# Kernel tuning notes

Hardware: AMD Instinct MI355X
Metric: run time of the kernel (lower is better)

## Reference

```python
import jax, jax.numpy as jnp
import numpy as np

EMB = 1024
HEADS = 16
HEAD_DIM = EMB // HEADS
FF = 4 * EMB


def _gelu_tanh(x):
    c = jnp.sqrt(jnp.asarray(2.0 / jnp.pi, x.dtype))
    return 0.5 * x * (1.0 + jnp.tanh(c * (x + 0.044715 * x ** 3)))


def _layernorm(x, scale, shift, eps=1e-5):
    mean = jnp.mean(x, axis=-1, keepdims=True)
    var = jnp.mean((x - mean) ** 2, axis=-1, keepdims=True)
    return scale * (x - mean) / jnp.sqrt(var + eps) + shift


def setup_inputs() -> dict:
    key = jax.random.key(0)
    ks = jax.random.split(key, 8)
    s = 0.02
    return {
        "x": jax.random.normal(ks[0], (2, 2048, EMB), jnp.float32),
        "w_q": jax.random.normal(ks[1], (EMB, EMB), jnp.float32) * s,
        "w_k": jax.random.normal(ks[2], (EMB, EMB), jnp.float32) * s,
        "w_v": jax.random.normal(ks[3], (EMB, EMB), jnp.float32) * s,
        "w_o": jax.random.normal(ks[4], (EMB, EMB), jnp.float32) * s,
        "b_o": jnp.zeros((EMB,), jnp.float32),
        "ln1_scale": jnp.ones((EMB,), jnp.float32),
        "ln1_shift": jnp.zeros((EMB,), jnp.float32),
        "ln2_scale": jnp.ones((EMB,), jnp.float32),
        "ln2_shift": jnp.zeros((EMB,), jnp.float32),
        "w_ff1": jax.random.normal(ks[5], (EMB, FF), jnp.float32) * s,
        "b_ff1": jnp.zeros((FF,), jnp.float32),
        "w_ff2": jax.random.normal(ks[6], (FF, EMB), jnp.float32) * s,
        "b_ff2": jnp.zeros((EMB,), jnp.float32),
    }


def _attention(x, w_q, w_k, w_v, w_o, b_o):
    b, n, _ = x.shape
    q = (x @ w_q).reshape(b, n, HEADS, HEAD_DIM).transpose(0, 2, 1, 3)  # bhnd
    k = (x @ w_k).reshape(b, n, HEADS, HEAD_DIM).transpose(0, 2, 1, 3)
    v = (x @ w_v).reshape(b, n, HEADS, HEAD_DIM).transpose(0, 2, 1, 3)
    scores = jnp.einsum("bhqd,bhkd->bhqk", q, k)
    causal = jnp.triu(jnp.ones((n, n), bool), k=1)
    scores = jnp.where(causal, -jnp.inf, scores)
    # original scales AFTER masking (-inf stays -inf)
    attn = jax.nn.softmax(scores / jnp.sqrt(jnp.asarray(HEAD_DIM, x.dtype)), axis=-1)
    ctx = jnp.einsum("bhqk,bhkd->bhqd", attn, v)
    ctx = ctx.transpose(0, 2, 1, 3).reshape(b, n, EMB)
    return ctx @ w_o + b_o


def reference(x, w_q, w_k, w_v, w_o, b_o, ln1_scale, ln1_shift,
              ln2_scale, ln2_shift, w_ff1, b_ff1, w_ff2, b_ff2):
    h = _layernorm(x, ln1_scale, ln1_shift)
    h = _attention(h, w_q, w_k, w_v, w_o, b_o)
    x = x + h  # dropout is identity at drop_rate=0 / eval
    h = _layernorm(x, ln2_scale, ln2_shift)
    h = _gelu_tanh(h @ w_ff1 + b_ff1) @ w_ff2 + b_ff2
    return x + h
```

## Files before the change

kernel.cpp:

```cpp
#include <hip/hip_runtime.h>
#include <math.h>

#define EMB 1024
#define HEADS 16
#define HD 64
#define FF_DIM 4096
#define SEQ 2048
#define BATCH 2
#define NTOK (BATCH * SEQ)

typedef __bf16 bf16x8 __attribute__((ext_vector_type(8)));
typedef float f32x4 __attribute__((ext_vector_type(4)));

__device__ __forceinline__ unsigned short f2bf(float f) {
    union { float f; unsigned int u; } v; v.f = f;
    unsigned int r = v.u + 0x7fff + ((v.u >> 16) & 1);
    return (unsigned short)(r >> 16);
}

__device__ __forceinline__ unsigned int cvt_pk_bf16(float a, float b) {
    unsigned int r;
    asm("v_cvt_pk_bf16_f32 %0, %1, %2" : "=v"(r) : "v"(a), "v"(b));
    return r;
}

__device__ __forceinline__ float gelu_f(float x) {
    const float A = 1.5957691216057308f;
    const float B = 0.07135481282989427f;
    float zz = x * (A + B * x * x);
    return x * __builtin_amdgcn_rcpf(1.f + __expf(-zz));
}

#define GLOAD_LDS16(g, l)                                                      \
    __builtin_amdgcn_global_load_lds(                                          \
        (const __attribute__((address_space(1))) void*)(g),                    \
        (__attribute__((address_space(3))) void*)(l), 16, 0, 0)

__global__ __launch_bounds__(256) void ln_kernel(const float* __restrict__ x,
                                                 const float* __restrict__ scale,
                                                 const float* __restrict__ shift,
                                                 unsigned short* __restrict__ out) {
    int row = blockIdx.x;
    const float* xr = x + (size_t)row * EMB;
    unsigned short* yr = out + (size_t)row * EMB;
    int t = threadIdx.x;

    float v[4];
    float s = 0.f, s2 = 0.f;
#pragma unroll
    for (int i = 0; i < 4; i++) {
        v[i] = xr[t + i * 256];
        s += v[i];
        s2 += v[i] * v[i];
    }
    for (int o = 32; o > 0; o >>= 1) {
        s += __shfl_down(s, o, 64);
        s2 += __shfl_down(s2, o, 64);
    }
    __shared__ float red[4], red2[4];
    int wave = t >> 6;
    if ((t & 63) == 0) { red[wave] = s; red2[wave] = s2; }
    __syncthreads();
    if (t == 0) {
        float a = 0.f, b = 0.f;
#pragma unroll
        for (int i = 0; i < 4; i++) { a += red[i]; b += red2[i]; }
        red[0] = a; red2[0] = b;
    }
    __syncthreads();
    float mean = red[0] * (1.f / EMB);
    float var = red2[0] * (1.f / EMB) - mean * mean;
    float rstd = rsqrtf(var + 1e-5f);
#pragma unroll
    for (int i = 0; i < 4; i++) {
        int c = t + i * 256;
        yr[c] = f2bf(scale[c] * (v[i] - mean) * rstd + shift[c]);
    }
}

__global__ __launch_bounds__(256) void prep_kernel(
    const float* __restrict__ w0, const float* __restrict__ w1,
    const float* __restrict__ w2, const float* __restrict__ w3,
    const float* __restrict__ w4, const float* __restrict__ w5,
    unsigned short* __restrict__ o0, unsigned short* __restrict__ o1,
    unsigned short* __restrict__ o2, unsigned short* __restrict__ o3,
    unsigned short* __restrict__ o4, unsigned short* __restrict__ o5,
    const float* __restrict__ x, const float* __restrict__ ln1s,
    const float* __restrict__ ln1b, unsigned short* __restrict__ lnO) {
    __shared__ float tile[64][65];
    __shared__ float red[4], red2[4];
    int id = blockIdx.x;
    int t = threadIdx.x;

    if (id >= 3072) {
        int row = id - 3072;
        const float* xr = x + (size_t)row * EMB;
        unsigned short* yr = lnO + (size_t)row * EMB;
        float v[4];
        float s = 0.f, s2 = 0.f;
#pragma unroll
        for (int i = 0; i < 4; i++) {
            v[i] = xr[t + i * 256];
            s += v[i];
            s2 += v[i] * v[i];
        }
        for (int o = 32; o > 0; o >>= 1) {
            s += __shfl_down(s, o, 64);
            s2 += __shfl_down(s2, o, 64);
        }
        int wave = t >> 6;
        if ((t & 63) == 0) { red[wave] = s; red2[wave] = s2; }
        __syncthreads();
        if (t == 0) {
            float a = 0.f, b = 0.f;
#pragma unroll
            for (int i = 0; i < 4; i++) { a += red[i]; b += red2[i]; }
            red[0] = a; red2[0] = b;
        }
        __syncthreads();
        float mean = red[0] * (1.f / EMB);
        float var = red2[0] * (1.f / EMB) - mean * mean;
        float rstd = rsqrtf(var + 1e-5f);
#pragma unroll
        for (int i = 0; i < 4; i++) {
            int c = t + i * 256;
            yr[c] = f2bf(ln1s[c] * (v[i] - mean) * rstd + ln1b[c]);
        }
        return;
    }

    const float* src; unsigned short* dst; int K, N, lid;
    if (id < 256)       { src = w0; dst = o0; K = 1024; N = 1024; lid = id; }
    else if (id < 512)  { src = w1; dst = o1; K = 1024; N = 1024; lid = id - 256; }
    else if (id < 768)  { src = w2; dst = o2; K = 1024; N = 1024; lid = id - 512; }
    else if (id < 1024) { src = w3; dst = o3; K = 1024; N = 1024; lid = id - 768; }
    else if (id < 2048) { src = w4; dst = o4; K = 1024; N = 4096; lid = id - 1024; }
    else                { src = w5; dst = o5; K = 4096; N = 1024; lid = id - 2048; }
    int tn = N >> 6;
    int k0 = (lid / tn) << 6, n0 = (lid % tn) << 6;
    int rr = t >> 6, cc = t & 63;
#pragma unroll
    for (int i = 0; i < 16; i++) {
        int r = i * 4 + rr;
        tile[r][cc] = src[(size_t)(k0 + r) * N + n0 + cc];
    }
    __syncthreads();
#pragma unroll
    for (int i = 0; i < 16; i++) {
        int r = i * 4 + rr;
        dst[(size_t)(n0 + r) * K + k0 + cc] = f2bf(tile[cc][r]);
    }
}


__global__ __launch_bounds__(256) void ff1_gemm(
    const unsigned short* __restrict__ A,
    const unsigned short* __restrict__ Bt,
    unsigned short* __restrict__ C,
    const float* __restrict__ bias,
    int M, int N, int K) {
    __shared__ unsigned short As[2][128 * 64];
    __shared__ unsigned short Bs[2][128 * 64];

    const int t = threadIdx.x;
    const int w = t >> 6, lane = t & 63;
    const int m0 = blockIdx.x * 128, n0 = blockIdx.y * 128;

    const int srow = lane >> 3;
    const int sc = (lane & 7) ^ srow;
    const unsigned short* gA[4];
    const unsigned short* gB[4];
#pragma unroll
    for (int i = 0; i < 4; i++) {
        gA[i] = A + (size_t)(m0 + i * 32 + w * 8 + srow) * K + sc * 8;
        gB[i] = Bt + (size_t)(n0 + i * 32 + w * 8 + srow) * K + sc * 8;
    }

    const int mrow = (w >> 1) * 64, ncol = (w & 1) * 64;
    int ph[2];
#pragma unroll
    for (int s = 0; s < 2; s++) ph[s] = ((s * 4 + (lane >> 4)) ^ (lane & 7)) * 8;
    int abase[4], bbase[4];
#pragma unroll
    for (int i = 0; i < 4; i++) {
        abase[i] = (mrow + i * 16 + (lane & 15)) * 64;
        bbase[i] = (ncol + i * 16 + (lane & 15)) * 64;
    }

    f32x4 acc[4][4];
#pragma unroll
    for (int i = 0; i < 4; i++)
#pragma unroll
        for (int j = 0; j < 4; j++) acc[i][j] = (f32x4){0.f, 0.f, 0.f, 0.f};

#define STG1(b)                                                                \
    do {                                                                       \
        _Pragma("unroll") for (int i_ = 0; i_ < 4; i_++) {                     \
            GLOAD_LDS16(gA[i_], &As[b][(i_ * 32 + w * 8) * 64]);               \
            GLOAD_LDS16(gB[i_], &Bs[b][(i_ * 32 + w * 8) * 64]);               \
            gA[i_] += 64; gB[i_] += 64;                                        \
        }                                                                      \
    } while (0)

    STG1(0);
    const int nk = K >> 6;
    for (int it = 0; it < nk; it++) {
        const int buf = it & 1;
        __syncthreads();
        if (it + 1 < nk) STG1(buf ^ 1);
#pragma unroll
        for (int s = 0; s < 2; s++) {
            bf16x8 af[4], bfr[4];
#pragma unroll
            for (int i = 0; i < 4; i++) {
                af[i] = *reinterpret_cast<const bf16x8*>(&As[buf][abase[i] + ph[s]]);
                bfr[i] = *reinterpret_cast<const bf16x8*>(&Bs[buf][bbase[i] + ph[s]]);
            }
#pragma unroll
            for (int i = 0; i < 4; i++)
#pragma unroll
                for (int j = 0; j < 4; j++)
                    acc[i][j] = __builtin_amdgcn_mfma_f32_16x16x32_bf16(
                        af[i], bfr[j], acc[i][j], 0, 0, 0);
        }
    }
#undef STG1

    const int ccol = lane & 15;
    const int crow = (lane >> 4) << 2;
#pragma unroll
    for (int i = 0; i < 4; i++) {
#pragma unroll
        for (int j = 0; j < 4; j++) {
            int col = n0 + ncol + j * 16 + ccol;
            float badd = bias[col];
#pragma unroll
            for (int r = 0; r < 4; r++) {
                int row = m0 + mrow + i * 16 + crow + r;
                C[(size_t)row * N + col] = f2bf(gelu_f(acc[i][j][r] + badd));
            }
        }
    }
}

__global__ __launch_bounds__(256) void ff2_gemm(
    const unsigned short* __restrict__ A,
    const unsigned short* __restrict__ Bt,
    float* __restrict__ C,
    const float* __restrict__ bias,
    int M, int N, int K) {
    __shared__ unsigned short As[2][128 * 64];
    __shared__ unsigned short Bs[2][128 * 64];

    const int t = threadIdx.x;
    const int w = t >> 6, lane = t & 63;
    const int id = blockIdx.x;
    const int n0 = (id & 7) * 128;
    const int ks = (id >> 3) & 1;
    const int m0 = (id >> 4) * 128;
    const int khalf = K >> 1;
    const int kbeg = ks * khalf;

    const int srow = lane >> 3;
    const int sc = (lane & 7) ^ srow;
    const unsigned short* gA[4];
    const unsigned short* gB[4];
#pragma unroll
    for (int i = 0; i < 4; i++) {
        gA[i] = A + (size_t)(m0 + i * 32 + w * 8 + srow) * K + kbeg + sc * 8;
        gB[i] = Bt + (size_t)(n0 + i * 32 + w * 8 + srow) * K + kbeg + sc * 8;
    }

    const int mrow = (w >> 1) * 64, ncol = (w & 1) * 64;
    int ph[2];
#pragma unroll
    for (int s = 0; s < 2; s++) ph[s] = ((s * 4 + (lane >> 4)) ^ (lane & 7)) * 8;
    int abase[4], bbase[4];
#pragma unroll
    for (int i = 0; i < 4; i++) {
        abase[i] = (mrow + i * 16 + (lane & 15)) * 64;
        bbase[i] = (ncol + i * 16 + (lane & 15)) * 64;
    }

    f32x4 acc[4][4];
#pragma unroll
    for (int i = 0; i < 4; i++)
#pragma unroll
        for (int j = 0; j < 4; j++) acc[i][j] = (f32x4){0.f, 0.f, 0.f, 0.f};

#define STG2(b)                                                                \
    do {                                                                       \
        _Pragma("unroll") for (int i_ = 0; i_ < 4; i_++) {                     \
            GLOAD_LDS16(gA[i_], &As[b][(i_ * 32 + w * 8) * 64]);               \
            GLOAD_LDS16(gB[i_], &Bs[b][(i_ * 32 + w * 8) * 64]);               \
            gA[i_] += 64; gB[i_] += 64;                                        \
        }                                                                      \
    } while (0)

    STG2(0);
    const int nk = khalf >> 6;
    for (int it = 0; it < nk; it++) {
        const int buf = it & 1;
        __syncthreads();
        if (it + 1 < nk) STG2(buf ^ 1);
#pragma unroll
        for (int s = 0; s < 2; s++) {
            bf16x8 af[4], bfr[4];
#pragma unroll
            for (int i = 0; i < 4; i++) {
                af[i] = *reinterpret_cast<const bf16x8*>(&As[buf][abase[i] + ph[s]]);
                bfr[i] = *reinterpret_cast<const bf16x8*>(&Bs[buf][bbase[i] + ph[s]]);
            }
#pragma unroll
            for (int i = 0; i < 4; i++)
#pragma unroll
                for (int j = 0; j < 4; j++)
                    acc[i][j] = __builtin_amdgcn_mfma_f32_16x16x32_bf16(
                        af[i], bfr[j], acc[i][j], 0, 0, 0);
        }
    }
#undef STG2

    const int ccol = lane & 15;
    const int crow = (lane >> 4) << 2;
#pragma unroll
    for (int i = 0; i < 4; i++) {
#pragma unroll
        for (int j = 0; j < 4; j++) {
            int col = n0 + ncol + j * 16 + ccol;
            float badd = ks == 0 ? bias[col] : 0.f;
#pragma unroll
            for (int r = 0; r < 4; r++) {
                int row = m0 + mrow + i * 16 + crow + r;
                size_t idx = (size_t)row * N + col;
                unsafeAtomicAdd(&C[idx], acc[i][j][r] + badd);
            }
        }
    }
}

template <int EPI>
__global__ __launch_bounds__(256) void mfma_gemm_s64(
    const unsigned short* __restrict__ A,
    const unsigned short* __restrict__ Bt,
    float* __restrict__ C,
    const float* __restrict__ bias,
    const float* __restrict__ resid,
    int M, int N, int K) {
    __shared__ unsigned short As[2][64 * 64];
    __shared__ unsigned short Bs[2][64 * 64];

    const int t = threadIdx.x;
    const int w = t >> 6, lane = t & 63;
    const int m0 = blockIdx.x * 64, n0 = blockIdx.y * 64;

    const int srow = lane >> 3;
    const int sc = (lane & 7) ^ srow;
    const unsigned short* gA[2];
    const unsigned short* gB[2];
#pragma unroll
    for (int i = 0; i < 2; i++) {
        gA[i] = A + (size_t)(m0 + i * 32 + w * 8 + srow) * K + sc * 8;
        gB[i] = Bt + (size_t)(n0 + i * 32 + w * 8 + srow) * K + sc * 8;
    }

    int ph[2];
#pragma unroll
    for (int s = 0; s < 2; s++) ph[s] = ((s * 4 + (lane >> 4)) ^ (lane & 7)) * 8;
    const int mrow = (w >> 1) * 32, ncol = (w & 1) * 32;
    int abase[2], bbase[2];
#pragma unroll
    for (int i = 0; i < 2; i++) {
        abase[i] = (mrow + i * 16 + (lane & 15)) * 64;
        bbase[i] = (ncol + i * 16 + (lane & 15)) * 64;
    }

    f32x4 acc[2][2];
#pragma unroll
    for (int i = 0; i < 2; i++)
#pragma unroll
        for (int j = 0; j < 2; j++) acc[i][j] = (f32x4){0.f, 0.f, 0.f, 0.f};

#define STGS(b)                                                                \
    do {                                                                       \
        _Pragma("unroll") for (int i_ = 0; i_ < 2; i_++) {                     \
            GLOAD_LDS16(gA[i_], &As[b][(i_ * 32 + w * 8) * 64]);               \
            GLOAD_LDS16(gB[i_], &Bs[b][(i_ * 32 + w * 8) * 64]);               \
            gA[i_] += 64; gB[i_] += 64;                                        \
        }                                                                      \
    } while (0)

    STGS(0);
    const int nk = K >> 6;
    for (int it = 0; it < nk; it++) {
        const int buf = it & 1;
        __syncthreads();
        if (it + 1 < nk) STGS(buf ^ 1);
#pragma unroll
        for (int s = 0; s < 2; s++) {
            bf16x8 af[2], bfr[2];
#pragma unroll
            for (int i = 0; i < 2; i++) {
                af[i] = *reinterpret_cast<const bf16x8*>(&As[buf][abase[i] + ph[s]]);
                bfr[i] = *reinterpret_cast<const bf16x8*>(&Bs[buf][bbase[i] + ph[s]]);
            }
#pragma unroll
            for (int i = 0; i < 2; i++)
#pragma unroll
                for (int j = 0; j < 2; j++)
                    acc[i][j] = __builtin_amdgcn_mfma_f32_16x16x32_bf16(
                        af[i], bfr[j], acc[i][j], 0, 0, 0);
        }
    }
#undef STGS

    const int ccol = lane & 15;
    const int crow = (lane >> 4) << 2;
#pragma unroll
    for (int i = 0; i < 2; i++) {
#pragma unroll
        for (int j = 0; j < 2; j++) {
            int col = n0 + ncol + j * 16 + ccol;
            float badd = bias[col];
#pragma unroll
            for (int r = 0; r < 4; r++) {
                int row = m0 + mrow + i * 16 + crow + r;
                size_t idx = (size_t)row * N + col;
                if constexpr (EPI == 1) {
                    C[idx] = acc[i][j][r] + badd + resid[idx];
                } else {
                    C[idx] = C[idx] + acc[i][j][r] + badd;
                }
            }
        }
    }
}

__global__ __launch_bounds__(256) void qkv_gemm(
    const unsigned short* __restrict__ lnO,
    const unsigned short* __restrict__ wqkT,
    const unsigned short* __restrict__ wvT,
    unsigned short* __restrict__ q,
    unsigned short* __restrict__ kb,
    unsigned short* __restrict__ vT) {
    __shared__ unsigned short As[2][128 * 64];
    __shared__ unsigned short Bs[2][128 * 64];

    const int t = threadIdx.x;
    const int w = t >> 6, lane = t & 63;
    const int bid = blockIdx.x;
    const bool qk = bid < 512;

    const unsigned short *A, *Bt;
    int m0, n0, N;
    if (qk) {
        A = lnO; Bt = wqkT;
        m0 = (bid & 31) * 128; n0 = (bid >> 5) * 128; N = 2048;
    } else {
        int lb = bid - 512;
        A = wvT; Bt = lnO;
        m0 = (lb & 7) * 128; n0 = (lb >> 3) * 128; N = 4096;
    }
    const int K = 1024;

    const int srow = lane >> 3;
    const int sc = (lane & 7) ^ srow;
    const unsigned short* gA[4];
    const unsigned short* gB[4];
#pragma unroll
    for (int i = 0; i < 4; i++) {
        gA[i] = A + (size_t)(m0 + i * 32 + w * 8 + srow) * K + sc * 8;
        gB[i] = Bt + (size_t)(n0 + i * 32 + w * 8 + srow) * K + sc * 8;
    }

    const int mrow = (w >> 1) * 64, ncol = (w & 1) * 64;
    int ph[2];
#pragma unroll
    for (int s = 0; s < 2; s++) ph[s] = ((s * 4 + (lane >> 4)) ^ (lane & 7)) * 8;
    int abase[4], bbase[4];
#pragma unroll
    for (int i = 0; i < 4; i++) {
        abase[i] = (mrow + i * 16 + (lane & 15)) * 64;
        bbase[i] = (ncol + i * 16 + (lane & 15)) * 64;
    }

    f32x4 acc[4][4];
#pragma unroll
    for (int i = 0; i < 4; i++)
#pragma unroll
        for (int j = 0; j < 4; j++) acc[i][j] = (f32x4){0.f, 0.f, 0.f, 0.f};

#define STGQ(b)                                                                \
    do {                                                                       \
        _Pragma("unroll") for (int i_ = 0; i_ < 4; i_++) {                     \
            GLOAD_LDS16(gA[i_], &As[b][(i_ * 32 + w * 8) * 64]);               \
            GLOAD_LDS16(gB[i_], &Bs[b][(i_ * 32 + w * 8) * 64]);               \
            gA[i_] += 64; gB[i_] += 64;                                        \
        }                                                                      \
    } while (0)

    STGQ(0);
    const int nk = K >> 6;
    for (int it = 0; it < nk; it++) {
        const int buf = it & 1;
        __syncthreads();
        if (it + 1 < nk) STGQ(buf ^ 1);
#pragma unroll
        for (int s = 0; s < 2; s++) {
            bf16x8 af[4], bfr[4];
#pragma unroll
            for (int i = 0; i < 4; i++) {
                af[i] = *reinterpret_cast<const bf16x8*>(&As[buf][abase[i] + ph[s]]);
                bfr[i] = *reinterpret_cast<const bf16x8*>(&Bs[buf][bbase[i] + ph[s]]);
            }
#pragma unroll
            for (int i = 0; i < 4; i++)
#pragma unroll
                for (int j = 0; j < 4; j++)
                    acc[i][j] = __builtin_amdgcn_mfma_f32_16x16x32_bf16(
                        af[i], bfr[j], acc[i][j], 0, 0, 0);
        }
    }
#undef STGQ

    const int ccol = lane & 15;
    const int crow = (lane >> 4) << 2;
    unsigned short* dst;
    int nbase;
    if (qk) {
        dst = (n0 < 1024) ? q : kb;
        nbase = n0 & 1023;
    } else {
        dst = vT;
        nbase = n0;
    }
    const int ldc = qk ? 1024 : 4096;
#pragma unroll
    for (int i = 0; i < 4; i++) {
#pragma unroll
        for (int j = 0; j < 4; j++) {
            int col = nbase + ncol + j * 16 + ccol;
#pragma unroll
            for (int r = 0; r < 4; r++) {
                int row = m0 + mrow + i * 16 + crow + r;
                dst[(size_t)row * ldc + col] = f2bf(acc[i][j][r]);
            }
        }
    }
}

__global__ __launch_bounds__(256) void attn_mfma(
    const unsigned short* __restrict__ Q,
    const unsigned short* __restrict__ K,
    const unsigned short* __restrict__ Vt,
    unsigned short* __restrict__ O) {
    __shared__ unsigned short Ks[2][64 * 64];
    __shared__ unsigned short Vs[2][64 * 64];
    __shared__ unsigned short Ps[4][16 * 64];

    const int t = threadIdx.x;
    const int w = t >> 6, lane = t & 63;
    const int l15 = lane & 15, l4 = lane >> 4;
    const int bh = blockIdx.x;
    const int b = bh >> 4, h = bh & 15;
    const int pair = blockIdx.y;

    const int sr = (w << 3) + (lane >> 3);
    const int sc = lane & 7;
    const int c = sc ^ (sr & 7);
    const unsigned short* kbase = K + ((size_t)(b * SEQ)) * EMB + h * HD;
    const unsigned short* vbase = Vt + ((size_t)(h * HD)) * (size_t)NTOK + (size_t)b * SEQ;
    unsigned short* Pw = &Ps[w][0];

#define STAGE(k0s, buf)                                                        \
    do {                                                                       \
        GLOAD_LDS16(kbase + (size_t)((k0s) + sr) * EMB + c * 8,                \
                    &Ks[buf][(w << 3) * 64]);                                  \
        GLOAD_LDS16(kbase + (size_t)((k0s) + sr + 32) * EMB + c * 8,           \
                    &Ks[buf][((w << 3) + 32) * 64]);                           \
        GLOAD_LDS16(vbase + (size_t)sr * NTOK + (k0s) + c * 8,                 \
                    &Vs[buf][(w << 3) * 64]);                                  \
        GLOAD_LDS16(vbase + (size_t)(sr + 32) * NTOK + (k0s) + c * 8,          \
                    &Vs[buf][((w << 3) + 32) * 64]);                           \
    } while (0)

    const float C1 = 0.125f * 1.4426950408889634f;
    const float C2 = 3.0f * 1.4426950408889634f;

#pragma unroll
    for (int phase = 0; phase < 2; phase++) {
        const int qt = phase ? pair : (31 - pair);
        const int q0 = qt * 64;

        const unsigned short* qg =
            Q + ((size_t)(b * SEQ + q0 + w * 16 + l15)) * EMB + h * HD + l4 * 8;
        bf16x8 qf0 = *(const bf16x8*)qg;
        bf16x8 qf1 = *(const bf16x8*)(qg + 32);
        const int qrow = q0 + w * 16 + l15;

        float ls[4] = {0.f, 0.f, 0.f, 0.f};
        f32x4 Oacc[4];
#pragma unroll
        for (int j = 0; j < 4; j++) Oacc[j] = (f32x4){0.f, 0.f, 0.f, 0.f};

        const int ntiles = qt + 1;
        __syncthreads();
        STAGE(0, 0);
        for (int tile = 0; tile < ntiles; tile++) {
            const int k0 = tile * 64;
            const int buf = tile & 1;
            __syncthreads();
            if (tile + 1 < ntiles) STAGE(k0 + 64, buf ^ 1);

            f32x4 S[4];
#pragma unroll
            for (int j = 0; j < 4; j++) S[j] = (f32x4){0.f, 0.f, 0.f, 0.f};
#pragma unroll
            for (int s = 0; s < 2; s++) {
                bf16x8 qf = s ? qf1 : qf0;
#pragma unroll
                for (int j = 0; j < 4; j++) {
                    int rk = 16 * j + l15;
                    int phys = (s * 4 + l4) ^ (rk & 7);
                    bf16x8 kf = *(const bf16x8*)&Ks[buf][rk * 64 + phys * 8];
                    S[j] = __builtin_amdgcn_mfma_f32_16x16x32_bf16(kf, qf, S[j], 0, 0, 0);
                }
            }

            if (tile == ntiles - 1) {
#pragma unroll
                for (int j = 0; j < 4; j++)
#pragma unroll
                    for (int r = 0; r < 4; r++) {
                        float e = exp2f(S[j][r] * C1 - C2);
                        if (k0 + 16 * j + 4 * l4 + r > qrow) e = 0.f;
                        S[j][r] = e;
                    }
            } else {
#pragma unroll
                for (int j = 0; j < 4; j++)
#pragma unroll
                    for (int r = 0; r < 4; r++)
                        S[j][r] = exp2f(S[j][r] * C1 - C2);
            }

#pragma unroll
            for (int j = 0; j < 4; j++) {
                ls[j] += S[j][0] + S[j][1] + S[j][2] + S[j][3];
                unsigned int lo = cvt_pk_bf16(S[j][0], S[j][1]);
                unsigned int hi = cvt_pk_bf16(S[j][2], S[j][3]);
                int chunk = (2 * j + (l4 >> 1)) ^ (l15 & 7);
                uint2 val; val.x = lo; val.y = hi;
                *reinterpret_cast<uint2*>(&Pw[l15 * 64 + chunk * 8 + (l4 & 1) * 4]) = val;
            }

#pragma unroll
            for (int s = 0; s < 2; s++) {
                int pch = (4 * s + l4) ^ (l15 & 7);
                bf16x8 pf = *(const bf16x8*)&Pw[l15 * 64 + pch * 8];
#pragma unroll
                for (int j = 0; j < 4; j++) {
                    int rv = 16 * j + l15;
                    int vph = (s * 4 + l4) ^ (rv & 7);
                    bf16x8 vf = *(const bf16x8*)&Vs[buf][rv * 64 + vph * 8];
                    Oacc[j] = __builtin_amdgcn_mfma_f32_16x16x32_bf16(vf, pf, Oacc[j], 0, 0, 0);
                }
            }
        }

        float l = ls[0] + ls[1] + ls[2] + ls[3];
        l += __shfl_xor(l, 16, 64);
        l += __shfl_xor(l, 32, 64);
        float inv = 1.f / l;
        size_t rowb = (size_t)(b * SEQ + qrow) * EMB + h * HD;
#pragma unroll
        for (int j = 0; j < 4; j++) {
            unsigned int lo = cvt_pk_bf16(Oacc[j][0] * inv, Oacc[j][1] * inv);
            unsigned int hi = cvt_pk_bf16(Oacc[j][2] * inv, Oacc[j][3] * inv);
            uint2 val; val.x = lo; val.y = hi;
            *reinterpret_cast<uint2*>(&O[rowb + 16 * j + 4 * l4]) = val;
        }
    }
#undef STAGE
}

extern "C" void kernel_launch(void* const* d_in, const int* in_sizes, int n_in,
                              void* d_out, int out_size, void* d_ws, size_t ws_size,
                              hipStream_t stream) {
    const float* x     = (const float*)d_in[0];
    const float* w_q   = (const float*)d_in[1];
    const float* w_k   = (const float*)d_in[2];
    const float* w_v   = (const float*)d_in[3];
    const float* w_o   = (const float*)d_in[4];
    const float* b_o   = (const float*)d_in[5];
    const float* ln1s  = (const float*)d_in[6];
    const float* ln1b  = (const float*)d_in[7];
    const float* ln2s  = (const float*)d_in[8];
    const float* ln2b  = (const float*)d_in[9];
    const float* w_ff1 = (const float*)d_in[10];
    const float* b_ff1 = (const float*)d_in[11];
    const float* w_ff2 = (const float*)d_in[12];
    const float* b_ff2 = (const float*)d_in[13];
    float* out = (float*)d_out;

    char* p = (char*)d_ws;
    unsigned short* lnO  = (unsigned short*)p; p += (size_t)NTOK * EMB * 2;
    unsigned short* q    = (unsigned short*)p; p += (size_t)NTOK * EMB * 2;
    unsigned short* kbuf = (unsigned short*)p; p += (size_t)NTOK * EMB * 2;
    unsigned short* vT   = (unsigned short*)p; p += (size_t)NTOK * EMB * 2;
    unsigned short* ctx  = (unsigned short*)p; p += (size_t)NTOK * EMB * 2;
    unsigned short* ff1a = (unsigned short*)p; p += (size_t)NTOK * FF_DIM * 2;
    unsigned short* wqkT = (unsigned short*)p; p += (size_t)2 * EMB * EMB * 2;
    unsigned short* wvT  = (unsigned short*)p; p += (size_t)EMB * EMB * 2;
    unsigned short* woT  = (unsigned short*)p; p += (size_t)EMB * EMB * 2;
    unsigned short* wf1T = (unsigned short*)p; p += (size_t)FF_DIM * EMB * 2;
    unsigned short* wf2T = (unsigned short*)p; p += (size_t)EMB * FF_DIM * 2;

    dim3 blk(256);
    dim3 gS64(NTOK / 64, EMB / 64);
    dim3 gFF1(NTOK / 128, FF_DIM / 128);
    dim3 gAttn(BATCH * HEADS, 16);

    prep_kernel<<<3072 + NTOK, blk, 0, stream>>>(
        w_q, w_k, w_v, w_o, w_ff1, w_ff2,
        wqkT, wqkT + (size_t)EMB * EMB, wvT, woT, wf1T, wf2T,
        x, ln1s, ln1b, lnO);
    qkv_gemm<<<768, blk, 0, stream>>>(lnO, wqkT, wvT, q, kbuf, vT);
    attn_mfma<<<gAttn, blk, 0, stream>>>(q, kbuf, vT, ctx);
    mfma_gemm_s64<1><<<gS64, blk, 0, stream>>>(ctx, woT, out, b_o, x, NTOK, EMB, EMB);
    ln_kernel<<<NTOK, blk, 0, stream>>>(out, ln2s, ln2b, ctx);
    ff1_gemm<<<gFF1, blk, 0, stream>>>(ctx, wf1T, ff1a, b_ff1, NTOK, FF_DIM, EMB);
    ff2_gemm<<<512, blk, 0, stream>>>(ff1a, wf2T, out, b_ff2, NTOK, EMB, FF_DIM);
}
```

Before: 338.5 us.

## Single-buffer LDS in GEMMs for occupancy and raise FF2 split-K to four

The qkv, ff1 and ff2 GEMM kernels drop LDS double buffering. Each now uses one 32KB A/B tile pair, loaded between two barriers per K step, so more blocks can be resident per CU and hide latency that way instead of by prefetching. The ff2 GEMM also goes from a 2-way to a 4-way K split, doubling its grid to 1024 blocks for more parallelism. The cost is lost load/compute overlap within a block, an extra barrier per iteration, and more partial-sum traffic for ff2.

After: 375.7 us. 1.11x slower.

```diff
diff --git a/kernel.cpp b/kernel.cpp
--- a/kernel.cpp
+++ b/kernel.cpp
@@ -159,8 +159,8 @@
     unsigned short* __restrict__ C,
     const float* __restrict__ bias,
     int M, int N, int K) {
-    __shared__ unsigned short As[2][128 * 64];
-    __shared__ unsigned short Bs[2][128 * 64];
+    __shared__ unsigned short As[128 * 64];
+    __shared__ unsigned short Bs[128 * 64];
 
     const int t = threadIdx.x;
     const int w = t >> 6, lane = t & 63;
@@ -193,28 +193,27 @@
 #pragma unroll
         for (int j = 0; j < 4; j++) acc[i][j] = (f32x4){0.f, 0.f, 0.f, 0.f};
 
-#define STG1(b)                                                                \
+#define STG1()                                                                 \
     do {                                                                       \
         _Pragma("unroll") for (int i_ = 0; i_ < 4; i_++) {                     \
-            GLOAD_LDS16(gA[i_], &As[b][(i_ * 32 + w * 8) * 64]);               \
-            GLOAD_LDS16(gB[i_], &Bs[b][(i_ * 32 + w * 8) * 64]);               \
+            GLOAD_LDS16(gA[i_], &As[(i_ * 32 + w * 8) * 64]);                  \
+            GLOAD_LDS16(gB[i_], &Bs[(i_ * 32 + w * 8) * 64]);                  \
             gA[i_] += 64; gB[i_] += 64;                                        \
         }                                                                      \
     } while (0)
 
-    STG1(0);
     const int nk = K >> 6;
     for (int it = 0; it < nk; it++) {
-        const int buf = it & 1;
-        __syncthreads();
-        if (it + 1 < nk) STG1(buf ^ 1);
+        __syncthreads();
+        STG1();
+        __syncthreads();
 #pragma unroll
         for (int s = 0; s < 2; s++) {
             bf16x8 af[4], bfr[4];
 #pragma unroll
             for (int i = 0; i < 4; i++) {
-                af[i] = *reinterpret_cast<const bf16x8*>(&As[buf][abase[i] + ph[s]]);
-                bfr[i] = *reinterpret_cast<const bf16x8*>(&Bs[buf][bbase[i] + ph[s]]);
+                af[i] = *reinterpret_cast<const bf16x8*>(&As[abase[i] + ph[s]]);
+                bfr[i] = *reinterpret_cast<const bf16x8*>(&Bs[bbase[i] + ph[s]]);
             }
 #pragma unroll
             for (int i = 0; i < 4; i++)
@@ -249,17 +248,17 @@
     float* __restrict__ C,
     const float* __restrict__ bias,
     int M, int N, int K) {
-    __shared__ unsigned short As[2][128 * 64];
-    __shared__ unsigned short Bs[2][128 * 64];
+    __shared__ unsigned short As[128 * 64];
+    __shared__ unsigned short Bs[128 * 64];
 
     const int t = threadIdx.x;
     const int w = t >> 6, lane = t & 63;
     const int id = blockIdx.x;
     const int n0 = (id & 7) * 128;
-    const int ks = (id >> 3) & 1;
-    const int m0 = (id >> 4) * 128;
-    const int khalf = K >> 1;
-    const int kbeg = ks * khalf;
+    const int ks = (id >> 3) & 3;
+    const int m0 = (id >> 5) * 128;
+    const int kq = K >> 2;
+    const int kbeg = ks * kq;
 
     const int srow = lane >> 3;
     const int sc = (lane & 7) ^ srow;
@@ -288,28 +287,27 @@
 #pragma unroll
         for (int j = 0; j < 4; j++) acc[i][j] = (f32x4){0.f, 0.f, 0.f, 0.f};
 
-#define STG2(b)                                                                \
+#define STG2()                                                                 \
     do {                                                                       \
         _Pragma("unroll") for (int i_ = 0; i_ < 4; i_++) {                     \
-            GLOAD_LDS16(gA[i_], &As[b][(i_ * 32 + w * 8) * 64]);               \
-            GLOAD_LDS16(gB[i_], &Bs[b][(i_ * 32 + w * 8) * 64]);               \
+            GLOAD_LDS16(gA[i_], &As[(i_ * 32 + w * 8) * 64]);                  \
+            GLOAD_LDS16(gB[i_], &Bs[(i_ * 32 + w * 8) * 64]);                  \
             gA[i_] += 64; gB[i_] += 64;                                        \
         }                                                                      \
     } while (0)
 
-    STG2(0);
-    const int nk = khalf >> 6;
+    const int nk = kq >> 6;
     for (int it = 0; it < nk; it++) {
-        const int buf = it & 1;
-        __syncthreads();
-        if (it + 1 < nk) STG2(buf ^ 1);
+        __syncthreads();
+        STG2();
+        __syncthreads();
 #pragma unroll
         for (int s = 0; s < 2; s++) {
             bf16x8 af[4], bfr[4];
 #pragma unroll
             for (int i = 0; i < 4; i++) {
-                af[i] = *reinterpret_cast<const bf16x8*>(&As[buf][abase[i] + ph[s]]);
-                bfr[i] = *reinterpret_cast<const bf16x8*>(&Bs[buf][bbase[i] + ph[s]]);
+                af[i] = *reinterpret_cast<const bf16x8*>(&As[abase[i] + ph[s]]);
+                bfr[i] = *reinterpret_cast<const bf16x8*>(&Bs[bbase[i] + ph[s]]);
             }
 #pragma unroll
             for (int i = 0; i < 4; i++)
@@ -443,8 +441,8 @@
     unsigned short* __restrict__ q,
     unsigned short* __restrict__ kb,
     unsigned short* __restrict__ vT) {
-    __shared__ unsigned short As[2][128 * 64];
-    __shared__ unsigned short Bs[2][128 * 64];
+    __shared__ unsigned short As[128 * 64];
+    __shared__ unsigned short Bs[128 * 64];
 
     const int t = threadIdx.x;
     const int w = t >> 6, lane = t & 63;
@@ -490,28 +488,27 @@
 #pragma unroll
         for (int j = 0; j < 4; j++) acc[i][j] = (f32x4){0.f, 0.f, 0.f, 0.f};
 
-#define STGQ(b)                                                                \
+#define STGQ()                                                                 \
     do {                                                                       \
         _Pragma("unroll") for (int i_ = 0; i_ < 4; i_++) {                     \
-            GLOAD_LDS16(gA[i_], &As[b][(i_ * 32 + w * 8) * 64]);               \
-            GLOAD_LDS16(gB[i_], &Bs[b][(i_ * 32 + w * 8) * 64]);               \
+            GLOAD_LDS16(gA[i_], &As[(i_ * 32 + w * 8) * 64]);                  \
+            GLOAD_LDS16(gB[i_], &Bs[(i_ * 32 + w * 8) * 64]);                  \
             gA[i_] += 64; gB[i_] += 64;                                        \
         }                                                                      \
     } while (0)
 
-    STGQ(0);
     const int nk = K >> 6;
     for (int it = 0; it < nk; it++) {
-        const int buf = it & 1;
-        __syncthreads();
-        if (it + 1 < nk) STGQ(buf ^ 1);
+        __syncthreads();
+        STGQ();
+        __syncthreads();
 #pragma unroll
         for (int s = 0; s < 2; s++) {
             bf16x8 af[4], bfr[4];
 #pragma unroll
             for (int i = 0; i < 4; i++) {
-                af[i] = *reinterpret_cast<const bf16x8*>(&As[buf][abase[i] + ph[s]]);
-                bfr[i] = *reinterpret_cast<const bf16x8*>(&Bs[buf][bbase[i] + ph[s]]);
+                af[i] = *reinterpret_cast<const bf16x8*>(&As[abase[i] + ph[s]]);
+                bfr[i] = *reinterpret_cast<const bf16x8*>(&Bs[bbase[i] + ph[s]]);
             }
 #pragma unroll
             for (int i = 0; i < 4; i++)
@@ -730,5 +727,5 @@
     mfma_gemm_s64<1><<<gS64, blk, 0, stream>>>(ctx, woT, out, b_o, x, NTOK, EMB, EMB);
     ln_kernel<<<NTOK, blk, 0, stream>>>(out, ln2s, ln2b, ctx);
     ff1_gemm<<<gFF1, blk, 0, stream>>>(ctx, wf1T, ff1a, b_ff1, NTOK, FF_DIM, EMB);
-    ff2_gemm<<<512, blk, 0, stream>>>(ff1a, wf2T, out, b_ff2, NTOK, EMB, FF_DIM);
-}
+    ff2_gemm<<<1024, blk, 0, stream>>>(ff1a, wf2T, out, b_ff2, NTOK, EMB, FF_DIM);
+}
```

## Halve GEMM K-tile to 32 with new LDS swizzle and 4-way split-K for FF2

Applied to the files above, without the earlier changes.

The three 128x128 MFMA GEMMs (QKV, FF1, FF2) now stage a K-depth of 32 per iteration instead of 64. This halves the LDS footprint from 64KB to 32KB per block, which should allow higher occupancy, and it uses a rotated 4-chunk swizzle in place of the XOR swizzle. FF2 moves from a 2-way to a 4-way K split with 1024 blocks, which adds parallelism but doubles the number of atomic or partial accumulations into the output. The cost is twice as many barriers and loop iterations per unit of work.

New measurement: 385.1 us. 13.8% more time.

```diff
diff --git a/kernel.cpp b/kernel.cpp
--- a/kernel.cpp
+++ b/kernel.cpp
@@ -159,32 +159,31 @@
     unsigned short* __restrict__ C,
     const float* __restrict__ bias,
     int M, int N, int K) {
-    __shared__ unsigned short As[2][128 * 64];
-    __shared__ unsigned short Bs[2][128 * 64];
+    __shared__ unsigned short As[2][128 * 32];
+    __shared__ unsigned short Bs[2][128 * 32];
 
     const int t = threadIdx.x;
     const int w = t >> 6, lane = t & 63;
+    const int l15 = lane & 15, l4 = lane >> 4;
     const int m0 = blockIdx.x * 128, n0 = blockIdx.y * 128;
 
-    const int srow = lane >> 3;
-    const int sc = (lane & 7) ^ srow;
-    const unsigned short* gA[4];
-    const unsigned short* gB[4];
+    const int sr = lane >> 2;
+    const int scn = ((lane & 3) - (lane >> 3)) & 3;
+    const unsigned short* gA[2];
+    const unsigned short* gB[2];
+#pragma unroll
+    for (int i = 0; i < 2; i++) {
+        gA[i] = A + (size_t)(m0 + 32 * w + 16 * i + sr) * K + scn * 8;
+        gB[i] = Bt + (size_t)(n0 + 32 * w + 16 * i + sr) * K + scn * 8;
+    }
+
+    const int mrow = (w >> 1) * 64, ncol = (w & 1) * 64;
+    const int pfr = (l4 + ((l15 >> 1) & 3)) & 3;
+    int abase[4], bbase[4];
 #pragma unroll
     for (int i = 0; i < 4; i++) {
-        gA[i] = A + (size_t)(m0 + i * 32 + w * 8 + srow) * K + sc * 8;
-        gB[i] = Bt + (size_t)(n0 + i * 32 + w * 8 + srow) * K + sc * 8;
-    }
-
-    const int mrow = (w >> 1) * 64, ncol = (w & 1) * 64;
-    int ph[2];
-#pragma unroll
-    for (int s = 0; s < 2; s++) ph[s] = ((s * 4 + (lane >> 4)) ^ (lane & 7)) * 8;
-    int abase[4], bbase[4];
-#pragma unroll
-    for (int i = 0; i < 4; i++) {
-        abase[i] = (mrow + i * 16 + (lane & 15)) * 64;
-        bbase[i] = (ncol + i * 16 + (lane & 15)) * 64;
+        abase[i] = (mrow + i * 16 + l15) * 32 + pfr * 8;
+        bbase[i] = (ncol + i * 16 + l15) * 32 + pfr * 8;
     }
 
     f32x4 acc[4][4];
@@ -195,39 +194,36 @@
 
 #define STG1(b)                                                                \
     do {                                                                       \
-        _Pragma("unroll") for (int i_ = 0; i_ < 4; i_++) {                     \
-            GLOAD_LDS16(gA[i_], &As[b][(i_ * 32 + w * 8) * 64]);               \
-            GLOAD_LDS16(gB[i_], &Bs[b][(i_ * 32 + w * 8) * 64]);               \
-            gA[i_] += 64; gB[i_] += 64;                                        \
+        _Pragma("unroll") for (int i_ = 0; i_ < 2; i_++) {                     \
+            GLOAD_LDS16(gA[i_], &As[b][(32 * w + 16 * i_) * 32]);              \
+            GLOAD_LDS16(gB[i_], &Bs[b][(32 * w + 16 * i_) * 32]);              \
+            gA[i_] += 32; gB[i_] += 32;                                        \
         }                                                                      \
     } while (0)
 
     STG1(0);
-    const int nk = K >> 6;
+    const int nk = K >> 5;
     for (int it = 0; it < nk; it++) {
         const int buf = it & 1;
         __syncthreads();
         if (it + 1 < nk) STG1(buf ^ 1);
-#pragma unroll
-        for (int s = 0; s < 2; s++) {
-            bf16x8 af[4], bfr[4];
-#pragma unroll
-            for (int i = 0; i < 4; i++) {
-                af[i] = *reinterpret_cast<const bf16x8*>(&As[buf][abase[i] + ph[s]]);
-                bfr[i] = *reinterpret_cast<const bf16x8*>(&Bs[buf][bbase[i] + ph[s]]);
-            }
-#pragma unroll
-            for (int i = 0; i < 4; i++)
-#pragma unroll
-                for (int j = 0; j < 4; j++)
-                    acc[i][j] = __builtin_amdgcn_mfma_f32_16x16x32_bf16(
-                        af[i], bfr[j], acc[i][j], 0, 0, 0);
-        }
+        bf16x8 af[4], bfr[4];
+#pragma unroll
+        for (int i = 0; i < 4; i++) {
+            af[i] = *reinterpret_cast<const bf16x8*>(&As[buf][abase[i]]);
+            bfr[i] = *reinterpret_cast<const bf16x8*>(&Bs[buf][bbase[i]]);
+        }
+#pragma unroll
+        for (int i = 0; i < 4; i++)
+#pragma unroll
+            for (int j = 0; j < 4; j++)
+                acc[i][j] = __builtin_amdgcn_mfma_f32_16x16x32_bf16(
+                    af[i], bfr[j], acc[i][j], 0, 0, 0);
     }
 #undef STG1
 
-    const int ccol = lane & 15;
-    const int crow = (lane >> 4) << 2;
+    const int ccol = l15;
+    const int crow = l4 << 2;
 #pragma unroll
     for (int i = 0; i < 4; i++) {
 #pragma unroll
@@ -249,37 +245,36 @@
     float* __restrict__ C,
     const float* __restrict__ bias,
     int M, int N, int K) {
-    __shared__ unsigned short As[2][128 * 64];
-    __shared__ unsigned short Bs[2][128 * 64];
+    __shared__ unsigned short As[2][128 * 32];
+    __shared__ unsigned short Bs[2][128 * 32];
 
     const int t = threadIdx.x;
     const int w = t >> 6, lane = t & 63;
+    const int l15 = lane & 15, l4 = lane >> 4;
     const int id = blockIdx.x;
     const int n0 = (id & 7) * 128;
-    const int ks = (id >> 3) & 1;
-    const int m0 = (id >> 4) * 128;
-    const int khalf = K >> 1;
-    const int kbeg = ks * khalf;
-
-    const int srow = lane >> 3;
-    const int sc = (lane & 7) ^ srow;
-    const unsigned short* gA[4];
-    const unsigned short* gB[4];
+    const int ks = (id >> 3) & 3;
+    const int m0 = (id >> 5) * 128;
+    const int kq = K >> 2;
+    const int kbeg = ks * kq;
+
+    const int sr = lane >> 2;
+    const int scn = ((lane & 3) - (lane >> 3)) & 3;
+    const unsigned short* gA[2];
+    const unsigned short* gB[2];
+#pragma unroll
+    for (int i = 0; i < 2; i++) {
+        gA[i] = A + (size_t)(m0 + 32 * w + 16 * i + sr) * K + kbeg + scn * 8;
+        gB[i] = Bt + (size_t)(n0 + 32 * w + 16 * i + sr) * K + kbeg + scn * 8;
+    }
+
+    const int mrow = (w >> 1) * 64, ncol = (w & 1) * 64;
+    const int pfr = (l4 + ((l15 >> 1) & 3)) & 3;
+    int abase[4], bbase[4];
 #pragma unroll
     for (int i = 0; i < 4; i++) {
-        gA[i] = A + (size_t)(m0 + i * 32 + w * 8 + srow) * K + kbeg + sc * 8;
-        gB[i] = Bt + (size_t)(n0 + i * 32 + w * 8 + srow) * K + kbeg + sc * 8;
-    }
-
-    const int mrow = (w >> 1) * 64, ncol = (w & 1) * 64;
-    int ph[2];
-#pragma unroll
-    for (int s = 0; s < 2; s++) ph[s] = ((s * 4 + (lane >> 4)) ^ (lane & 7)) * 8;
-    int abase[4], bbase[4];
-#pragma unroll
-    for (int i = 0; i < 4; i++) {
-        abase[i] = (mrow + i * 16 + (lane & 15)) * 64;
-        bbase[i] = (ncol + i * 16 + (lane & 15)) * 64;
+        abase[i] = (mrow + i * 16 + l15) * 32 + pfr * 8;
+        bbase[i] = (ncol + i * 16 + l15) * 32 + pfr * 8;
     }
 
     f32x4 acc[4][4];
@@ -290,39 +285,36 @@
 
 #define STG2(b)                                                                \
     do {                                                                       \
-        _Pragma("unroll") for (int i_ = 0; i_ < 4; i_++) {                     \
-            GLOAD_LDS16(gA[i_], &As[b][(i_ * 32 + w * 8) * 64]);               \
-            GLOAD_LDS16(gB[i_], &Bs[b][(i_ * 32 + w * 8) * 64]);               \
-            gA[i_] += 64; gB[i_] += 64;                                        \
+        _Pragma("unroll") for (int i_ = 0; i_ < 2; i_++) {                     \
+            GLOAD_LDS16(gA[i_], &As[b][(32 * w + 16 * i_) * 32]);              \
+            GLOAD_LDS16(gB[i_], &Bs[b][(32 * w + 16 * i_) * 32]);              \
+            gA[i_] += 32; gB[i_] += 32;                                        \
         }                                                                      \
     } while (0)
 
     STG2(0);
-    const int nk = khalf >> 6;
+    const int nk = kq >> 5;
     for (int it = 0; it < nk; it++) {
         const int buf = it & 1;
         __syncthreads();
         if (it + 1 < nk) STG2(buf ^ 1);
-#pragma unroll
-        for (int s = 0; s < 2; s++) {
-            bf16x8 af[4], bfr[4];
-#pragma unroll
-            for (int i = 0; i < 4; i++) {
-                af[i] = *reinterpret_cast<const bf16x8*>(&As[buf][abase[i] + ph[s]]);
-                bfr[i] = *reinterpret_cast<const bf16x8*>(&Bs[buf][bbase[i] + ph[s]]);
-            }
-#pragma unroll
-            for (int i = 0; i < 4; i++)
-#pragma unroll
-                for (int j = 0; j < 4; j++)
-                    acc[i][j] = __builtin_amdgcn_mfma_f32_16x16x32_bf16(
-                        af[i], bfr[j], acc[i][j], 0, 0, 0);
-        }
+        bf16x8 af[4], bfr[4];
+#pragma unroll
+        for (int i = 0; i < 4; i++) {
+            af[i] = *reinterpret_cast<const bf16x8*>(&As[buf][abase[i]]);
+            bfr[i] = *reinterpret_cast<const bf16x8*>(&Bs[buf][bbase[i]]);
+        }
+#pragma unroll
+        for (int i = 0; i < 4; i++)
+#pragma unroll
+            for (int j = 0; j < 4; j++)
+                acc[i][j] = __builtin_amdgcn_mfma_f32_16x16x32_bf16(
+                    af[i], bfr[j], acc[i][j], 0, 0, 0);
     }
 #undef STG2
 
-    const int ccol = lane & 15;
-    const int crow = (lane >> 4) << 2;
+    const int ccol = l15;
+    const int crow = l4 << 2;
 #pragma unroll
     for (int i = 0; i < 4; i++) {
 #pragma unroll
@@ -443,11 +435,12 @@
     unsigned short* __restrict__ q,
     unsigned short* __restrict__ kb,
     unsigned short* __restrict__ vT) {
-    __shared__ unsigned short As[2][128 * 64];
-    __shared__ unsigned short Bs[2][128 * 64];
+    __shared__ unsigned short As[2][128 * 32];
+    __shared__ unsigned short Bs[2][128 * 32];
 
     const int t = threadIdx.x;
     const int w = t >> 6, lane = t & 63;
+    const int l15 = lane & 15, l4 = lane >> 4;
     const int bid = blockIdx.x;
     const bool qk = bid < 512;
 
@@ -463,25 +456,23 @@
     }
     const int K = 1024;
 
-    const int srow = lane >> 3;
-    const int sc = (lane & 7) ^ srow;
-    const unsigned short* gA[4];
-    const unsigned short* gB[4];
+    const int sr = lane >> 2;
+    const int scn = ((lane & 3) - (lane >> 3)) & 3;
+    const unsigned short* gA[2];
+    const unsigned short* gB[2];
+#pragma unroll
+    for (int i = 0; i < 2; i++) {
+        gA[i] = A + (size_t)(m0 + 32 * w + 16 * i + sr) * K + scn * 8;
+        gB[i] = Bt + (size_t)(n0 + 32 * w + 16 * i + sr) * K + scn * 8;
+    }
+
+    const int mrow = (w >> 1) * 64, ncol = (w & 1) * 64;
+    const int pfr = (l4 + ((l15 >> 1) & 3)) & 3;
+    int abase[4], bbase[4];
 #pragma unroll
     for (int i = 0; i < 4; i++) {
-        gA[i] = A + (size_t)(m0 + i * 32 + w * 8 + srow) * K + sc * 8;
-        gB[i] = Bt + (size_t)(n0 + i * 32 + w * 8 + srow) * K + sc * 8;
-    }
-
-    const int mrow = (w >> 1) * 64, ncol = (w & 1) * 64;
-    int ph[2];
-#pragma unroll
-    for (int s = 0; s < 2; s++) ph[s] = ((s * 4 + (lane >> 4)) ^ (lane & 7)) * 8;
-    int abase[4], bbase[4];
-#pragma unroll
-    for (int i = 0; i < 4; i++) {
-        abase[i] = (mrow + i * 16 + (lane & 15)) * 64;
-        bbase[i] = (ncol + i * 16 + (lane & 15)) * 64;
+        abase[i] = (mrow + i * 16 + l15) * 32 + pfr * 8;
+        bbase[i] = (ncol + i * 16 + l15) * 32 + pfr * 8;
     }
 
     f32x4 acc[4][4];
@@ -492,39 +483,36 @@
 
 #define STGQ(b)                                                                \
     do {                                                                       \
-        _Pragma("unroll") for (int i_ = 0; i_ < 4; i_++) {                     \
-            GLOAD_LDS16(gA[i_], &As[b][(i_ * 32 + w * 8) * 64]);               \
-            GLOAD_LDS16(gB[i_], &Bs[b][(i_ * 32 + w * 8) * 64]);               \
-            gA[i_] += 64; gB[i_] += 64;                                        \
+        _Pragma("unroll") for (int i_ = 0; i_ < 2; i_++) {                     \
+            GLOAD_LDS16(gA[i_], &As[b][(32 * w + 16 * i_) * 32]);              \
+            GLOAD_LDS16(gB[i_], &Bs[b][(32 * w + 16 * i_) * 32]);              \
+            gA[i_] += 32; gB[i_] += 32;                                        \
         }                                                                      \
     } while (0)
 
     STGQ(0);
-    const int nk = K >> 6;
+    const int nk = K >> 5;
     for (int it = 0; it < nk; it++) {
         const int buf = it & 1;
         __syncthreads();
         if (it + 1 < nk) STGQ(buf ^ 1);
-#pragma unroll
-        for (int s = 0; s < 2; s++) {
-            bf16x8 af[4], bfr[4];
-#pragma unroll
-            for (int i = 0; i < 4; i++) {
-                af[i] = *reinterpret_cast<const bf16x8*>(&As[buf][abase[i] + ph[s]]);
-                bfr[i] = *reinterpret_cast<const bf16x8*>(&Bs[buf][bbase[i] + ph[s]]);
-            }
-#pragma unroll
-            for (int i = 0; i < 4; i++)
-#pragma unroll
-                for (int j = 0; j < 4; j++)
-                    acc[i][j] = __builtin_amdgcn_mfma_f32_16x16x32_bf16(
-                        af[i], bfr[j], acc[i][j], 0, 0, 0);
-        }
+        bf16x8 af[4], bfr[4];
+#pragma unroll
+        for (int i = 0; i < 4; i++) {
+            af[i] = *reinterpret_cast<const bf16x8*>(&As[buf][abase[i]]);
+            bfr[i] = *reinterpret_cast<const bf16x8*>(&Bs[buf][bbase[i]]);
+        }
+#pragma unroll
+        for (int i = 0; i < 4; i++)
+#pragma unroll
+            for (int j = 0; j < 4; j++)
+                acc[i][j] = __builtin_amdgcn_mfma_f32_16x16x32_bf16(
+                    af[i], bfr[j], acc[i][j], 0, 0, 0);
     }
 #undef STGQ
 
-    const int ccol = lane & 15;
-    const int crow = (lane >> 4) << 2;
+    const int ccol = l15;
+    const int crow = l4 << 2;
     unsigned short* dst;
     int nbase;
     if (qk) {
@@ -730,5 +718,5 @@
     mfma_gemm_s64<1><<<gS64, blk, 0, stream>>>(ctx, woT, out, b_o, x, NTOK, EMB, EMB);
     ln_kernel<<<NTOK, blk, 0, stream>>>(out, ln2s, ln2b, ctx);
     ff1_gemm<<<gFF1, blk, 0, stream>>>(ctx, wf1T, ff1a, b_ff1, NTOK, FF_DIM, EMB);
-    ff2_gemm<<<512, blk, 0, stream>>>(ff1a, wf2T, out, b_ff2, NTOK, EMB, FF_DIM);
-}
+    ff2_gemm<<<1024, blk, 0, stream>>>(ff1a, wf2T, out, b_ff2, NTOK, EMB, FF_DIM);
+}
```
